# Optimization experiments

Measured on AMD Instinct MI355X. Metric: run time of the kernel, lower is better.

The kernel has to match this reference:

```python
import jax, jax.numpy as jnp
import numpy as np

N_NODES = 50000
N_EDGES = 1600000
NFEAT, NHID, NCLASS = 256, 128, 40
DROPOUT_P = 0.5


def gcn_conv(x, W, b, src, dst, n):
    # PyG GCNConv: h = X W; add self-loops; symmetric norm D^-1/2 (A+I) D^-1/2.
    h = x @ W  # [N, out]
    loop = jnp.arange(n, dtype=src.dtype)
    s = jnp.concatenate([src, loop])  # [E+N]
    d = jnp.concatenate([dst, loop])
    deg = jax.ops.segment_sum(jnp.ones_like(d, dtype=h.dtype), d, num_segments=n)  # in-degree incl. self-loop
    dinv = jax.lax.rsqrt(jnp.maximum(deg, 1.0))
    norm = dinv[s] * dinv[d]  # [E+N]
    msg = h[s] * norm[:, None]  # [E+N, out] gather
    out = jax.ops.segment_sum(msg, d, num_segments=n)  # scatter-add
    return out + b


def setup_inputs() -> dict:
    key = jax.random.key(0)
    k = jax.random.split(key, 7)
    x = jax.random.normal(k[0], (N_NODES, NFEAT), dtype=jnp.float32)
    edge_index = jax.random.randint(k[1], (2, N_EDGES), 0, N_NODES, dtype=jnp.int64)
    W1 = jax.random.normal(k[2], (NFEAT, NHID), dtype=jnp.float32) * (1.0 / np.sqrt(NFEAT))
    b1 = jnp.zeros((NHID,), dtype=jnp.float32)
    W2 = jax.random.normal(k[3], (NHID, NCLASS), dtype=jnp.float32) * (1.0 / np.sqrt(NHID))
    b2 = jnp.zeros((NCLASS,), dtype=jnp.float32)
    keep = jax.random.bernoulli(k[4], 1.0 - DROPOUT_P, (N_NODES, NHID))
    drop_mask = keep.astype(jnp.float32) / (1.0 - DROPOUT_P)  # fixed training-mode dropout mask
    return {"x": x, "edge_index": edge_index, "W1": W1, "b1": b1, "W2": W2, "b2": b2, "drop_mask": drop_mask}


def reference(x, edge_index, W1, b1, W2, b2, drop_mask):
    src, dst = edge_index[0], edge_index[1]
    h = gcn_conv(x, W1, b1, src, dst, N_NODES)
    h = jax.nn.relu(h)
    h = h * drop_mask  # F.dropout(training=True) with fixed mask
    h = gcn_conv(h, W2, b2, src, dst, N_NODES)
    return jax.nn.log_softmax(h, axis=1)
```

## Files before the change

### kernel.cpp

```cpp
#include <hip/hip_runtime.h>
#include <hip/hip_fp16.h>
#include <math.h>

#define N_NODES 50000
#define N_EDGES 1600000
#define NFEAT 256
#define NHID 128
#define NCLASS 40

#define BSHIFT 7
#define NBUCK 391
#define CAP 5120
#define EPB 4096

typedef _Float16 f16x8 __attribute__((ext_vector_type(8)));
typedef float f32x4 __attribute__((ext_vector_type(4)));

__global__ __launch_bounds__(256) void k_binA(const int* __restrict__ src,
                                              const int* __restrict__ dst,
                                              int* __restrict__ gcur,
                                              unsigned int* __restrict__ packed) {
    __shared__ int lhist[NBUCK];
    __shared__ int lbase[NBUCK];
    __shared__ int lcur[NBUCK];
    int t = threadIdx.x;
    for (int i = t; i < NBUCK; i += 256) { lhist[i] = 0; lcur[i] = 0; }
    __syncthreads();
    int e0 = blockIdx.x * EPB;
    int e1 = min(e0 + EPB, N_EDGES);
    for (int e = e0 + t; e < e1; e += 256) {
        int b = dst[e] >> BSHIFT;
        atomicAdd(&lhist[b], 1);
    }
    __syncthreads();
    for (int i = t; i < NBUCK; i += 256)
        lbase[i] = atomicAdd(&gcur[i], lhist[i]);
    __syncthreads();
    for (int e = e0 + t; e < e1; e += 256) {
        int d = dst[e];
        int b = d >> BSHIFT;
        int r = atomicAdd(&lcur[b], 1);
        int pos = lbase[b] + r;
        if (pos < CAP)
            packed[(size_t)b * CAP + pos] =
                ((unsigned int)src[e] << BSHIFT) | (unsigned int)(d & 127);
    }
}

__global__ __launch_bounds__(256) void k_binB(const int* __restrict__ gcur,
                                              const unsigned int* __restrict__ packed,
                                              int* __restrict__ esrc,
                                              int* __restrict__ row_beg,
                                              int* __restrict__ row_cnt,
                                              float* __restrict__ dinv) {
    __shared__ unsigned int sp[CAP];
    __shared__ int hist[128];
    __shared__ int scan[128];
    __shared__ int cur[128];
    int b = blockIdx.x;
    int t = threadIdx.x;
    int cnt = min(gcur[b], CAP);
    if (t < 128) { hist[t] = 0; cur[t] = 0; }
    __syncthreads();
    const unsigned int* pin = packed + (size_t)b * CAP;
    for (int i = t; i < cnt; i += 256) {
        unsigned int w = pin[i];
        sp[i] = w;
        atomicAdd(&hist[w & 127], 1);
    }
    __syncthreads();
    if (t == 0) {
        int s = 0;
        for (int i = 0; i < 128; i++) { scan[i] = s; s += hist[i]; }
    }
    __syncthreads();
    for (int i = t; i < cnt; i += 256) {
        unsigned int w = sp[i];
        int dl = (int)(w & 127u);
        int r = atomicAdd(&cur[dl], 1);
        esrc[(size_t)b * CAP + scan[dl] + r] = (int)(w >> BSHIFT);
    }
    if (t < 128) {
        int node = b * 128 + t;
        if (node < N_NODES) {
            row_beg[node] = b * CAP + scan[t];
            row_cnt[node] = hist[t];
            dinv[node] = rsqrtf((float)(hist[t] + 1));
        }
    }
}

__global__ __launch_bounds__(256) void k_prep(const float* __restrict__ W1,
                                              const float* __restrict__ W2,
                                              __half* __restrict__ w1t,
                                              __half* __restrict__ w2t,
                                              int* __restrict__ gcur) {
    int t = blockIdx.x * 256 + threadIdx.x;
    if (t < NBUCK) gcur[t] = 0;
    if (t < 128 * 256) {
        int n = t >> 8, k = t & 255;
        w1t[t] = __float2half(W1[k * NHID + n]);
    }
    if (t < 48 * 128) {
        int n = t >> 7, k = t & 127;
        w2t[t] = __float2half(n < NCLASS ? W2[k * NCLASS + n] : 0.0f);
    }
}

#define G1_LDA 72
#define G1_LDB 72
#define G1_LDE 136
__global__ __launch_bounds__(256) void k_gemm1(const float* __restrict__ x,
                                               const __half* __restrict__ w1t,
                                               __half* __restrict__ h1h) {
    __shared__ __half smem[64 * G1_LDA + 128 * G1_LDB];
    __half* sA = smem;
    __half* sB = smem + 64 * G1_LDA;
    int t = threadIdx.x;
    int rbase = blockIdx.x * 64;
    int lane = t & 63, wv = t >> 6;
    int m = lane & 15, quad = lane >> 4;
    f32x4 acc[8];
    #pragma unroll
    for (int i = 0; i < 8; i++) acc[i] = (f32x4)0.0f;

    int arow = t >> 2, aseg = t & 3;
    int grow = rbase + arow;
    bool avalid = grow < N_NODES;
    int bn = t >> 1, bseg = t & 1;

    for (int k0 = 0; k0 < NFEAT; k0 += 64) {
        const float4* gs = (const float4*)(x + (size_t)grow * NFEAT + k0 + aseg * 16);
        __half* ad = sA + arow * G1_LDA + aseg * 16;
        #pragma unroll
        for (int i = 0; i < 4; i++) {
            float4 v = avalid ? gs[i] : make_float4(0.f, 0.f, 0.f, 0.f);
            __half2 h0 = __float22half2_rn(make_float2(v.x, v.y));
            __half2 h1 = __float22half2_rn(make_float2(v.z, v.w));
            uint2 st;
            st.x = __builtin_bit_cast(unsigned int, h0);
            st.y = __builtin_bit_cast(unsigned int, h1);
            *(uint2*)(ad + i * 4) = st;
        }
        const uint4* ws4 = (const uint4*)(w1t + bn * NFEAT + k0 + bseg * 32);
        uint4* bd = (uint4*)(sB + bn * G1_LDB + bseg * 32);
        #pragma unroll
        for (int i = 0; i < 4; i++) bd[i] = ws4[i];
        __syncthreads();
        #pragma unroll
        for (int kk = 0; kk < 64; kk += 32) {
            f16x8 af = *(const f16x8*)(sA + (wv * 16 + m) * G1_LDA + kk + quad * 8);
            #pragma unroll
            for (int t8 = 0; t8 < 8; t8++) {
                f16x8 bf = *(const f16x8*)(sB + (t8 * 16 + m) * G1_LDB + kk + quad * 8);
                acc[t8] = __builtin_amdgcn_mfma_f32_16x16x32_f16(af, bf, acc[t8], 0, 0, 0);
            }
        }
        __syncthreads();
    }
    __half* eb = smem;
    #pragma unroll
    for (int t8 = 0; t8 < 8; t8++) {
        #pragma unroll
        for (int r = 0; r < 4; r++)
            eb[(wv * 16 + quad * 4 + r) * G1_LDE + t8 * 16 + m] = __float2half(acc[t8][r]);
    }
    __syncthreads();
    if (avalid) {
        const uint4* es = (const uint4*)(eb + arow * G1_LDE + aseg * 32);
        uint4* od = (uint4*)(h1h + (size_t)grow * NHID + aseg * 32);
        #pragma unroll
        for (int i = 0; i < 4; i++) od[i] = es[i];
    }
}

#define G2_LDA 136
#define G2_LDB 136
#define G2_LDE 72
__global__ __launch_bounds__(256) void k_gemm2(const __half* __restrict__ h1p,
                                               const __half* __restrict__ w2t,
                                               __half* __restrict__ h2p) {
    __shared__ __half smem[64 * G2_LDA + 48 * G2_LDB];
    __half* sA = smem;
    __half* sB = smem + 64 * G2_LDA;
    int t = threadIdx.x;
    int rbase = blockIdx.x * 64;
    int lane = t & 63, wv = t >> 6;
    int m = lane & 15, quad = lane >> 4;
    f32x4 acc[3];
    #pragma unroll
    for (int i = 0; i < 3; i++) acc[i] = (f32x4)0.0f;

    int arow = t >> 2, aseg = t & 3;
    int grow = rbase + arow;
    bool avalid = grow < N_NODES;

    #pragma unroll
    for (int i = 0; i < 3; i++) {
        int idx = t + i * 256;
        int n = idx >> 4, seg = idx & 15;
        *(uint4*)(sB + n * G2_LDB + seg * 8) = *(const uint4*)(w2t + n * NHID + seg * 8);
    }
    {
        const uint4* gs = (const uint4*)(h1p + (size_t)grow * NHID + aseg * 32);
        uint4* ad = (uint4*)(sA + arow * G2_LDA + aseg * 32);
        uint4 z; z.x = z.y = z.z = z.w = 0;
        #pragma unroll
        for (int i = 0; i < 4; i++) ad[i] = avalid ? gs[i] : z;
    }
    __syncthreads();
    #pragma unroll
    for (int kk = 0; kk < 128; kk += 32) {
        f16x8 af = *(const f16x8*)(sA + (wv * 16 + m) * G2_LDA + kk + quad * 8);
        #pragma unroll
        for (int t3 = 0; t3 < 3; t3++) {
            f16x8 bf = *(const f16x8*)(sB + (t3 * 16 + m) * G2_LDB + kk + quad * 8);
            acc[t3] = __builtin_amdgcn_mfma_f32_16x16x32_f16(af, bf, acc[t3], 0, 0, 0);
        }
    }
    __syncthreads();
    __half* eb = smem;
    #pragma unroll
    for (int t3 = 0; t3 < 3; t3++) {
        #pragma unroll
        for (int r = 0; r < 4; r++)
            eb[(wv * 16 + quad * 4 + r) * G2_LDE + t3 * 16 + m] = __float2half(acc[t3][r]);
    }
    {
        int zr = t >> 2, zc = 48 + (t & 3) * 4;
        uint2 z; z.x = z.y = 0;
        *(uint2*)(eb + zr * G2_LDE + zc) = z;
    }
    __syncthreads();
    #pragma unroll
    for (int i = 0; i < 2; i++) {
        int idx = t + i * 256;
        int row = idx >> 3, seg = idx & 7;
        int gr = rbase + row;
        if (gr < N_NODES)
            *(uint4*)(h2p + (size_t)gr * 64 + seg * 8) = *(const uint4*)(eb + row * G2_LDE + seg * 8);
    }
}

__device__ __forceinline__ void acc8f(float* acc, uint4 v, float d) {
    float2 a0 = __half22float2(__builtin_bit_cast(__half2, v.x));
    float2 a1 = __half22float2(__builtin_bit_cast(__half2, v.y));
    float2 a2 = __half22float2(__builtin_bit_cast(__half2, v.z));
    float2 a3 = __half22float2(__builtin_bit_cast(__half2, v.w));
    acc[0] = fmaf(a0.x, d, acc[0]); acc[1] = fmaf(a0.y, d, acc[1]);
    acc[2] = fmaf(a1.x, d, acc[2]); acc[3] = fmaf(a1.y, d, acc[3]);
    acc[4] = fmaf(a2.x, d, acc[4]); acc[5] = fmaf(a2.y, d, acc[5]);
    acc[6] = fmaf(a3.x, d, acc[6]); acc[7] = fmaf(a3.y, d, acc[7]);
}

__global__ __launch_bounds__(64) void k_agg1(const __half* __restrict__ h1h,
                                             const float* __restrict__ dinv,
                                             const int* __restrict__ row_beg,
                                             const int* __restrict__ row_cnt,
                                             const int* __restrict__ esrc,
                                             const float* __restrict__ b1,
                                             const float* __restrict__ mask,
                                             __half* __restrict__ h1p) {
    int i = blockIdx.x;
    int lane = threadIdx.x;
    int q = lane >> 4;
    int fl = lane & 15;
    const uint4* hv4 = (const uint4*)h1h;
    float di = dinv[i];
    __half2 hacc[4];
    __half2 hz = __half2half2(__float2half(0.0f));
    hacc[0] = hz; hacc[1] = hz; hacc[2] = hz; hacc[3] = hz;
    int s0 = row_beg[i], cnt = row_cnt[i];
    for (int base = 0; base < cnt; base += 64) {
        int idx = base + lane;
        int sv = (idx < cnt) ? esrc[s0 + idx] : 0;
        float dv = (idx < cnt) ? dinv[sv] : 0.0f;
        int n = min(64, cnt - base);
        int nr = (n + 31) & ~31;
        for (int j = 0; j < nr; j += 32) {
            int ss[8]; __half2 dd[8]; uint4 vv[8];
            #pragma unroll
            for (int k = 0; k < 8; k++) {
                int jx = j + 4 * k + q;
                ss[k] = __shfl(sv, jx);
                float df = __shfl(dv, jx);
                dd[k] = __half2half2(__float2half(df));
            }
            #pragma unroll
            for (int k = 0; k < 8; k++) vv[k] = hv4[(size_t)ss[k] * 16 + fl];
            #pragma unroll
            for (int k = 0; k < 8; k++) {
                hacc[0] = __hfma2(__builtin_bit_cast(__half2, vv[k].x), dd[k], hacc[0]);
                hacc[1] = __hfma2(__builtin_bit_cast(__half2, vv[k].y), dd[k], hacc[1]);
                hacc[2] = __hfma2(__builtin_bit_cast(__half2, vv[k].z), dd[k], hacc[2]);
                hacc[3] = __hfma2(__builtin_bit_cast(__half2, vv[k].w), dd[k], hacc[3]);
            }
        }
    }
    float acc[8];
    #pragma unroll
    for (int k2 = 0; k2 < 4; k2++) {
        float2 f = __half22float2(hacc[k2]);
        acc[2 * k2] = f.x; acc[2 * k2 + 1] = f.y;
    }
    #pragma unroll
    for (int k = 0; k < 8; k++) {
        acc[k] += __shfl_xor(acc[k], 16);
        acc[k] += __shfl_xor(acc[k], 32);
    }
    if (q == 0) {
        uint4 sv4 = hv4[(size_t)i * 16 + fl];
        acc8f(acc, sv4, di);
        float4 bb0 = ((const float4*)b1)[fl * 2];
        float4 bb1 = ((const float4*)b1)[fl * 2 + 1];
        const float4* mrow = (const float4*)(mask + (size_t)i * NHID);
        float4 mm0 = mrow[fl * 2];
        float4 mm1 = mrow[fl * 2 + 1];
        float o0 = fmaxf(fmaf(acc[0], di, bb0.x), 0.f) * mm0.x;
        float o1 = fmaxf(fmaf(acc[1], di, bb0.y), 0.f) * mm0.y;
        float o2 = fmaxf(fmaf(acc[2], di, bb0.z), 0.f) * mm0.z;
        float o3 = fmaxf(fmaf(acc[3], di, bb0.w), 0.f) * mm0.w;
        float o4 = fmaxf(fmaf(acc[4], di, bb1.x), 0.f) * mm1.x;
        float o5 = fmaxf(fmaf(acc[5], di, bb1.y), 0.f) * mm1.y;
        float o6 = fmaxf(fmaf(acc[6], di, bb1.z), 0.f) * mm1.z;
        float o7 = fmaxf(fmaf(acc[7], di, bb1.w), 0.f) * mm1.w;
        __half2 p0 = __float22half2_rn(make_float2(o0, o1));
        __half2 p1 = __float22half2_rn(make_float2(o2, o3));
        __half2 p2 = __float22half2_rn(make_float2(o4, o5));
        __half2 p3 = __float22half2_rn(make_float2(o6, o7));
        uint4 st;
        st.x = __builtin_bit_cast(unsigned int, p0);
        st.y = __builtin_bit_cast(unsigned int, p1);
        st.z = __builtin_bit_cast(unsigned int, p2);
        st.w = __builtin_bit_cast(unsigned int, p3);
        ((uint4*)h1p)[(size_t)i * 16 + fl] = st;
    }
}

__global__ __launch_bounds__(64) void k_agg2(const __half* __restrict__ h2p,
                                             const float* __restrict__ dinv,
                                             const int* __restrict__ row_beg,
                                             const int* __restrict__ row_cnt,
                                             const int* __restrict__ esrc,
                                             const float* __restrict__ b2,
                                             float* __restrict__ out) {
    int i = blockIdx.x;
    int lane = threadIdx.x;
    int o8 = lane >> 3;
    int fl = lane & 7;
    const uint4* hv4 = (const uint4*)h2p;
    float di = dinv[i];
    __half2 hacc[4];
    __half2 hz = __half2half2(__float2half(0.0f));
    hacc[0] = hz; hacc[1] = hz; hacc[2] = hz; hacc[3] = hz;
    int s0 = row_beg[i], cnt = row_cnt[i];
    for (int base = 0; base < cnt; base += 64) {
        int idx = base + lane;
        int sv = (idx < cnt) ? esrc[s0 + idx] : 0;
        float dv = (idx < cnt) ? dinv[sv] : 0.0f;
        int n = min(64, cnt - base);
        int nr = (n + 31) & ~31;
        for (int j = 0; j < nr; j += 32) {
            int ss[4]; __half2 dd[4]; uint4 vv[4];
            #pragma unroll
            for (int k = 0; k < 4; k++) {
                int jx = j + 8 * k + o8;
                ss[k] = __shfl(sv, jx);
                float df = __shfl(dv, jx);
                dd[k] = __half2half2(__float2half(df));
            }
            #pragma unroll
            for (int k = 0; k < 4; k++) vv[k] = hv4[(size_t)ss[k] * 8 + fl];
            #pragma unroll
            for (int k = 0; k < 4; k++) {
                hacc[0] = __hfma2(__builtin_bit_cast(__half2, vv[k].x), dd[k], hacc[0]);
                hacc[1] = __hfma2(__builtin_bit_cast(__half2, vv[k].y), dd[k], hacc[1]);
                hacc[2] = __hfma2(__builtin_bit_cast(__half2, vv[k].z), dd[k], hacc[2]);
                hacc[3] = __hfma2(__builtin_bit_cast(__half2, vv[k].w), dd[k], hacc[3]);
            }
        }
    }
    float acc[8];
    #pragma unroll
    for (int k2 = 0; k2 < 4; k2++) {
        float2 f = __half22float2(hacc[k2]);
        acc[2 * k2] = f.x; acc[2 * k2 + 1] = f.y;
    }
    if (o8 == 0) {
        uint4 sv4 = hv4[(size_t)i * 8 + fl];
        acc8f(acc, sv4, di);
    }
    #pragma unroll
    for (int k = 0; k < 8; k++) {
        acc[k] += __shfl_xor(acc[k], 8);
        acc[k] += __shfl_xor(acc[k], 16);
        acc[k] += __shfl_xor(acc[k], 32);
    }
    if (o8 == 0) {
        bool act = (fl < 5);
        float val[8];
        float m = -INFINITY;
        if (act) {
            float4 bb0 = ((const float4*)b2)[fl * 2];
            float4 bb1 = ((const float4*)b2)[fl * 2 + 1];
            val[0] = fmaf(acc[0], di, bb0.x);
            val[1] = fmaf(acc[1], di, bb0.y);
            val[2] = fmaf(acc[2], di, bb0.z);
            val[3] = fmaf(acc[3], di, bb0.w);
            val[4] = fmaf(acc[4], di, bb1.x);
            val[5] = fmaf(acc[5], di, bb1.y);
            val[6] = fmaf(acc[6], di, bb1.z);
            val[7] = fmaf(acc[7], di, bb1.w);
            #pragma unroll
            for (int k = 0; k < 8; k++) m = fmaxf(m, val[k]);
        }
        m = fmaxf(m, __shfl_xor(m, 1));
        m = fmaxf(m, __shfl_xor(m, 2));
        m = fmaxf(m, __shfl_xor(m, 4));
        float ss = 0.f;
        if (act) {
            #pragma unroll
            for (int k = 0; k < 8; k++) ss += expf(val[k] - m);
        }
        ss += __shfl_xor(ss, 1);
        ss += __shfl_xor(ss, 2);
        ss += __shfl_xor(ss, 4);
        if (act) {
            float ls = m + logf(ss);
            float4 r0 = make_float4(val[0] - ls, val[1] - ls, val[2] - ls, val[3] - ls);
            float4 r1 = make_float4(val[4] - ls, val[5] - ls, val[6] - ls, val[7] - ls);
            float4* orow = (float4*)(out + (size_t)i * NCLASS + fl * 8);
            orow[0] = r0;
            orow[1] = r1;
        }
    }
}

extern "C" void kernel_launch(void* const* d_in, const int* in_sizes, int n_in,
                              void* d_out, int out_size, void* d_ws, size_t ws_size,
                              hipStream_t stream) {
    const float* x    = (const float*)d_in[0];
    const int*   ei   = (const int*)d_in[1];
    const float* W1   = (const float*)d_in[2];
    const float* b1   = (const float*)d_in[3];
    const float* W2   = (const float*)d_in[4];
    const float* b2   = (const float*)d_in[5];
    const float* mask = (const float*)d_in[6];
    float* out = (float*)d_out;

    const int* src = ei;
    const int* dst = ei + N_EDGES;

    char* ws = (char*)d_ws;
    size_t off = 0;
    __half* h1p    = (__half*)(ws + off); off += (size_t)N_NODES * NHID * 2;
    __half* h1h    = (__half*)(ws + off); off += (size_t)N_NODES * NHID * 2;
    int*    esrc   = (int*)   (ws + off); off += (size_t)NBUCK * CAP * 4;
    float*  dinv   = (float*) (ws + off); off += 200192;
    int*   row_beg = (int*)   (ws + off); off += 200192;
    int*   row_cnt = (int*)   (ws + off); off += 200192;
    int*   gcur    = (int*)   (ws + off); off += 2048;
    __half* w1t    = (__half*)(ws + off); off += 128 * 256 * 2;
    __half* w2t    = (__half*)(ws + off); off += 48 * 128 * 2;

    unsigned int* packed = (unsigned int*)h1p;
    __half* h2p = h1h;

    k_prep<<<128, 256, 0, stream>>>(W1, W2, w1t, w2t, gcur);
    k_binA<<<(N_EDGES + EPB - 1) / EPB, 256, 0, stream>>>(src, dst, gcur, packed);
    k_binB<<<NBUCK, 256, 0, stream>>>(gcur, packed, esrc, row_beg, row_cnt, dinv);

    k_gemm1<<<(N_NODES + 63) / 64, 256, 0, stream>>>(x, w1t, h1h);
    k_agg1<<<N_NODES, 64, 0, stream>>>(h1h, dinv, row_beg, row_cnt, esrc, b1, mask, h1p);
    k_gemm2<<<(N_NODES + 63) / 64, 256, 0, stream>>>(h1p, w2t, h2p);
    k_agg2<<<N_NODES, 64, 0, stream>>>(h2p, dinv, row_beg, row_cnt, esrc, b2, out);
}
```

Baseline: 266.8 us.

## Compact edge indices to 16-bit, shrink bins, and store layer-2 features unpadded

Edge source ids are now stored as unsigned short instead of int, since node ids fit in 16 bits; this halves CSR index traffic in both aggregation kernels. Binning uses 64-node buckets with smaller per-bucket capacity, which reduces shared memory in the second binning pass. The layer-2 hidden matrix is written with a 40-half row stride instead of padding to 64, so agg2 gathers 5 vector loads per neighbour instead of 8 and leaves three lanes per group idle. The main risk is bucket overflow, since each bucket now has less absolute slack above its expected edge count.

```diff
diff --git a/kernel.cpp b/kernel.cpp
--- a/kernel.cpp
+++ b/kernel.cpp
@@ -8,10 +8,10 @@
 #define NHID 128
 #define NCLASS 40
 
-#define BSHIFT 7
-#define NBUCK 391
-#define CAP 5120
-#define EPB 4096
+#define BSHIFT 6
+#define NBUCK 782
+#define CAP 2560
+#define EPB 2048
 
 typedef _Float16 f16x8 __attribute__((ext_vector_type(8)));
 typedef float f32x4 __attribute__((ext_vector_type(4)));
@@ -43,45 +43,45 @@
         int pos = lbase[b] + r;
         if (pos < CAP)
             packed[(size_t)b * CAP + pos] =
-                ((unsigned int)src[e] << BSHIFT) | (unsigned int)(d & 127);
+                ((unsigned int)src[e] << BSHIFT) | (unsigned int)(d & 63);
     }
 }
 
 __global__ __launch_bounds__(256) void k_binB(const int* __restrict__ gcur,
                                               const unsigned int* __restrict__ packed,
-                                              int* __restrict__ esrc,
+                                              unsigned short* __restrict__ esrc,
                                               int* __restrict__ row_beg,
                                               int* __restrict__ row_cnt,
                                               float* __restrict__ dinv) {
     __shared__ unsigned int sp[CAP];
-    __shared__ int hist[128];
-    __shared__ int scan[128];
-    __shared__ int cur[128];
+    __shared__ int hist[64];
+    __shared__ int scan[64];
+    __shared__ int cur[64];
     int b = blockIdx.x;
     int t = threadIdx.x;
     int cnt = min(gcur[b], CAP);
-    if (t < 128) { hist[t] = 0; cur[t] = 0; }
+    if (t < 64) { hist[t] = 0; cur[t] = 0; }
     __syncthreads();
     const unsigned int* pin = packed + (size_t)b * CAP;
     for (int i = t; i < cnt; i += 256) {
         unsigned int w = pin[i];
         sp[i] = w;
-        atomicAdd(&hist[w & 127], 1);
+        atomicAdd(&hist[w & 63], 1);
     }
     __syncthreads();
     if (t == 0) {
         int s = 0;
-        for (int i = 0; i < 128; i++) { scan[i] = s; s += hist[i]; }
+        for (int i = 0; i < 64; i++) { scan[i] = s; s += hist[i]; }
     }
     __syncthreads();
     for (int i = t; i < cnt; i += 256) {
         unsigned int w = sp[i];
-        int dl = (int)(w & 127u);
+        int dl = (int)(w & 63u);
         int r = atomicAdd(&cur[dl], 1);
-        esrc[(size_t)b * CAP + scan[dl] + r] = (int)(w >> BSHIFT);
-    }
-    if (t < 128) {
-        int node = b * 128 + t;
+        esrc[(size_t)b * CAP + scan[dl] + r] = (unsigned short)(w >> BSHIFT);
+    }
+    if (t < 64) {
+        int node = b * 64 + t;
         if (node < N_NODES) {
             row_beg[node] = b * CAP + scan[t];
             row_cnt[node] = hist[t];
@@ -176,7 +176,7 @@
 
 #define G2_LDA 136
 #define G2_LDB 136
-#define G2_LDE 72
+#define G2_LDE 40
 __global__ __launch_bounds__(256) void k_gemm2(const __half* __restrict__ h1p,
                                                const __half* __restrict__ w2t,
                                                __half* __restrict__ h2p) {
@@ -222,23 +222,20 @@
     __half* eb = smem;
     #pragma unroll
     for (int t3 = 0; t3 < 3; t3++) {
-        #pragma unroll
-        for (int r = 0; r < 4; r++)
-            eb[(wv * 16 + quad * 4 + r) * G2_LDE + t3 * 16 + m] = __float2half(acc[t3][r]);
-    }
-    {
-        int zr = t >> 2, zc = 48 + (t & 3) * 4;
-        uint2 z; z.x = z.y = 0;
-        *(uint2*)(eb + zr * G2_LDE + zc) = z;
-    }
-    __syncthreads();
-    #pragma unroll
-    for (int i = 0; i < 2; i++) {
-        int idx = t + i * 256;
-        int row = idx >> 3, seg = idx & 7;
+        int col = t3 * 16 + m;
+        if (col < NCLASS) {
+            #pragma unroll
+            for (int r = 0; r < 4; r++)
+                eb[(wv * 16 + quad * 4 + r) * G2_LDE + col] = __float2half(acc[t3][r]);
+        }
+    }
+    __syncthreads();
+    for (int idx = t; idx < 320; idx += 256) {
+        int row = idx / 5, seg = idx % 5;
         int gr = rbase + row;
         if (gr < N_NODES)
-            *(uint4*)(h2p + (size_t)gr * 64 + seg * 8) = *(const uint4*)(eb + row * G2_LDE + seg * 8);
+            *(uint4*)(h2p + (size_t)gr * G2_LDE + seg * 8) =
+                *(const uint4*)(eb + row * G2_LDE + seg * 8);
     }
 }
 
@@ -257,7 +254,7 @@
                                              const float* __restrict__ dinv,
                                              const int* __restrict__ row_beg,
                                              const int* __restrict__ row_cnt,
-                                             const int* __restrict__ esrc,
+                                             const unsigned short* __restrict__ esrc,
                                              const float* __restrict__ b1,
                                              const float* __restrict__ mask,
                                              __half* __restrict__ h1p) {
@@ -273,7 +270,7 @@
     int s0 = row_beg[i], cnt = row_cnt[i];
     for (int base = 0; base < cnt; base += 64) {
         int idx = base + lane;
-        int sv = (idx < cnt) ? esrc[s0 + idx] : 0;
+        int sv = (idx < cnt) ? (int)esrc[s0 + idx] : 0;
         float dv = (idx < cnt) ? dinv[sv] : 0.0f;
         int n = min(64, cnt - base);
         int nr = (n + 31) & ~31;
@@ -341,22 +338,24 @@
                                              const float* __restrict__ dinv,
                                              const int* __restrict__ row_beg,
                                              const int* __restrict__ row_cnt,
-                                             const int* __restrict__ esrc,
+                                             const unsigned short* __restrict__ esrc,
                                              const float* __restrict__ b2,
                                              float* __restrict__ out) {
     int i = blockIdx.x;
     int lane = threadIdx.x;
     int o8 = lane >> 3;
     int fl = lane & 7;
+    bool gact = fl < 5;
     const uint4* hv4 = (const uint4*)h2p;
     float di = dinv[i];
     __half2 hacc[4];
     __half2 hz = __half2half2(__float2half(0.0f));
     hacc[0] = hz; hacc[1] = hz; hacc[2] = hz; hacc[3] = hz;
     int s0 = row_beg[i], cnt = row_cnt[i];
+    uint4 zero4; zero4.x = zero4.y = zero4.z = zero4.w = 0;
     for (int base = 0; base < cnt; base += 64) {
         int idx = base + lane;
-        int sv = (idx < cnt) ? esrc[s0 + idx] : 0;
+        int sv = (idx < cnt) ? (int)esrc[s0 + idx] : 0;
         float dv = (idx < cnt) ? dinv[sv] : 0.0f;
         int n = min(64, cnt - base);
         int nr = (n + 31) & ~31;
@@ -370,7 +369,7 @@
                 dd[k] = __half2half2(__float2half(df));
             }
             #pragma unroll
-            for (int k = 0; k < 4; k++) vv[k] = hv4[(size_t)ss[k] * 8 + fl];
+            for (int k = 0; k < 4; k++) vv[k] = gact ? hv4[(size_t)ss[k] * 5 + fl] : zero4;
             #pragma unroll
             for (int k = 0; k < 4; k++) {
                 hacc[0] = __hfma2(__builtin_bit_cast(__half2, vv[k].x), dd[k], hacc[0]);
@@ -386,8 +385,8 @@
         float2 f = __half22float2(hacc[k2]);
         acc[2 * k2] = f.x; acc[2 * k2 + 1] = f.y;
     }
-    if (o8 == 0) {
-        uint4 sv4 = hv4[(size_t)i * 8 + fl];
+    if (o8 == 0 && gact) {
+        uint4 sv4 = hv4[(size_t)i * 5 + fl];
         acc8f(acc, sv4, di);
     }
     #pragma unroll
@@ -455,11 +454,12 @@
     size_t off = 0;
     __half* h1p    = (__half*)(ws + off); off += (size_t)N_NODES * NHID * 2;
     __half* h1h    = (__half*)(ws + off); off += (size_t)N_NODES * NHID * 2;
-    int*    esrc   = (int*)   (ws + off); off += (size_t)NBUCK * CAP * 4;
+    unsigned short* esrc = (unsigned short*)(ws + off);
+    off += ((size_t)NBUCK * CAP * 2 + 255) & ~(size_t)255;
     float*  dinv   = (float*) (ws + off); off += 200192;
     int*   row_beg = (int*)   (ws + off); off += 200192;
     int*   row_cnt = (int*)   (ws + off); off += 200192;
-    int*   gcur    = (int*)   (ws + off); off += 2048;
+    int*   gcur    = (int*)   (ws + off); off += 4096;
     __half* w1t    = (__half*)(ws + off); off += 128 * 256 * 2;
     __half* w2t    = (__half*)(ws + off); off += 48 * 128 * 2;
 
```

Result: slower. 282.2 us (+5.7%).

## Segment edges by source range and batch 64 nodes per agg1 block

Applied to the files above, without the earlier changes.

k_binB now sorts each bucket's edges twice. One order groups them by source-node segment (4 ranges of 12800 nodes) and then by destination row. The other is the plain per-row order used by k_agg2. Edge source indices are stored as 16-bit values, halving index traffic. k_agg1 now runs 256-thread blocks covering 64 nodes, with 4 nodes per 16-lane group, walking the segments in order. The aim is to keep the gathered h1 rows within a smaller working set that stays in cache. In exchange, binning does more work, k_agg1 keeps fewer loads in flight per group, and segment locality only holds if blocks progress roughly in step.

```diff
diff --git a/kernel.cpp b/kernel.cpp
--- a/kernel.cpp
+++ b/kernel.cpp
@@ -12,6 +12,8 @@
 #define NBUCK 391
 #define CAP 5120
 #define EPB 4096
+#define SEGN 4
+#define SEGSZ 12800
 
 typedef _Float16 f16x8 __attribute__((ext_vector_type(8)));
 typedef float f32x4 __attribute__((ext_vector_type(4)));
@@ -49,44 +51,89 @@
 
 __global__ __launch_bounds__(256) void k_binB(const int* __restrict__ gcur,
                                               const unsigned int* __restrict__ packed,
-                                              int* __restrict__ esrc,
+                                              unsigned short* __restrict__ esrc_seg,
+                                              unsigned short* __restrict__ esrc_row,
+                                              int* __restrict__ sbeg,
+                                              int* __restrict__ scnt,
                                               int* __restrict__ row_beg,
                                               int* __restrict__ row_cnt,
                                               float* __restrict__ dinv) {
     __shared__ unsigned int sp[CAP];
-    __shared__ int hist[128];
-    __shared__ int scan[128];
-    __shared__ int cur[128];
+    __shared__ int hist[512];
+    __shared__ int scan[512];
+    __shared__ int cur[512];
+    __shared__ int psum[64];
     int b = blockIdx.x;
     int t = threadIdx.x;
     int cnt = min(gcur[b], CAP);
-    if (t < 128) { hist[t] = 0; cur[t] = 0; }
+    for (int i = t; i < 512; i += 256) { hist[i] = 0; cur[i] = 0; }
     __syncthreads();
     const unsigned int* pin = packed + (size_t)b * CAP;
     for (int i = t; i < cnt; i += 256) {
         unsigned int w = pin[i];
         sp[i] = w;
-        atomicAdd(&hist[w & 127], 1);
+        int srcv = (int)(w >> BSHIFT);
+        atomicAdd(&hist[(srcv / SEGSZ) * 128 + (int)(w & 127u)], 1);
+    }
+    __syncthreads();
+    if (t < 64) {
+        int s = 0;
+        #pragma unroll
+        for (int j = 0; j < 8; j++) s += hist[t * 8 + j];
+        psum[t] = s;
     }
     __syncthreads();
     if (t == 0) {
         int s = 0;
-        for (int i = 0; i < 128; i++) { scan[i] = s; s += hist[i]; }
+        for (int j = 0; j < 64; j++) { int v = psum[j]; psum[j] = s; s += v; }
+    }
+    __syncthreads();
+    if (t < 64) {
+        int s = psum[t];
+        #pragma unroll
+        for (int j = 0; j < 8; j++) { scan[t * 8 + j] = s; s += hist[t * 8 + j]; }
+    }
+    __syncthreads();
+    for (int i = t; i < cnt; i += 256) {
+        unsigned int w = sp[i];
+        int srcv = (int)(w >> BSHIFT);
+        int key = (srcv / SEGSZ) * 128 + (int)(w & 127u);
+        int r = atomicAdd(&cur[key], 1);
+        esrc_seg[(size_t)b * CAP + scan[key] + r] = (unsigned short)srcv;
+    }
+    if (t < 128) {
+        int node = b * 128 + t;
+        if (node < N_NODES) {
+            int tot = 0;
+            #pragma unroll
+            for (int s = 0; s < SEGN; s++) {
+                sbeg[node * 4 + s] = b * CAP + scan[s * 128 + t];
+                scnt[node * 4 + s] = hist[s * 128 + t];
+                tot += hist[s * 128 + t];
+            }
+            row_cnt[node] = tot;
+            dinv[node] = rsqrtf((float)(tot + 1));
+        }
+    }
+    __syncthreads();
+    if (t < 128) { hist[t] = 0; cur[t] = 0; }
+    __syncthreads();
+    for (int i = t; i < cnt; i += 256) atomicAdd(&hist[sp[i] & 127u], 1);
+    __syncthreads();
+    if (t == 0) {
+        int s = 0;
+        for (int j = 0; j < 128; j++) { int v = hist[j]; scan[j] = s; s += v; }
     }
     __syncthreads();
     for (int i = t; i < cnt; i += 256) {
         unsigned int w = sp[i];
         int dl = (int)(w & 127u);
         int r = atomicAdd(&cur[dl], 1);
-        esrc[(size_t)b * CAP + scan[dl] + r] = (int)(w >> BSHIFT);
+        esrc_row[(size_t)b * CAP + scan[dl] + r] = (unsigned short)(w >> BSHIFT);
     }
     if (t < 128) {
         int node = b * 128 + t;
-        if (node < N_NODES) {
-            row_beg[node] = b * CAP + scan[t];
-            row_cnt[node] = hist[t];
-            dinv[node] = rsqrtf((float)(hist[t] + 1));
-        }
+        if (node < N_NODES) row_beg[node] = b * CAP + scan[t];
     }
 }
 
@@ -253,69 +300,89 @@
     acc[6] = fmaf(a3.x, d, acc[6]); acc[7] = fmaf(a3.y, d, acc[7]);
 }
 
-__global__ __launch_bounds__(64) void k_agg1(const __half* __restrict__ h1h,
-                                             const float* __restrict__ dinv,
-                                             const int* __restrict__ row_beg,
-                                             const int* __restrict__ row_cnt,
-                                             const int* __restrict__ esrc,
-                                             const float* __restrict__ b1,
-                                             const float* __restrict__ mask,
-                                             __half* __restrict__ h1p) {
-    int i = blockIdx.x;
-    int lane = threadIdx.x;
-    int q = lane >> 4;
-    int fl = lane & 15;
+__global__ __launch_bounds__(256) void k_agg1(const __half* __restrict__ h1h,
+                                              const float* __restrict__ dinv,
+                                              const int* __restrict__ sbeg,
+                                              const int* __restrict__ scnt,
+                                              const unsigned short* __restrict__ esrc_seg,
+                                              const float* __restrict__ b1,
+                                              const float* __restrict__ mask,
+                                              __half* __restrict__ h1p) {
+    int t = threadIdx.x;
+    int qw = t >> 4, ln = t & 15;
+    int nbase = blockIdx.x * 64;
     const uint4* hv4 = (const uint4*)h1h;
-    float di = dinv[i];
-    __half2 hacc[4];
+    __half2 hacc[4][4];
     __half2 hz = __half2half2(__float2half(0.0f));
-    hacc[0] = hz; hacc[1] = hz; hacc[2] = hz; hacc[3] = hz;
-    int s0 = row_beg[i], cnt = row_cnt[i];
-    for (int base = 0; base < cnt; base += 64) {
-        int idx = base + lane;
-        int sv = (idx < cnt) ? esrc[s0 + idx] : 0;
-        float dv = (idx < cnt) ? dinv[sv] : 0.0f;
-        int n = min(64, cnt - base);
-        int nr = (n + 31) & ~31;
-        for (int j = 0; j < nr; j += 32) {
-            int ss[8]; __half2 dd[8]; uint4 vv[8];
-            #pragma unroll
-            for (int k = 0; k < 8; k++) {
-                int jx = j + 4 * k + q;
-                ss[k] = __shfl(sv, jx);
-                float df = __shfl(dv, jx);
-                dd[k] = __half2half2(__float2half(df));
+    #pragma unroll
+    for (int k = 0; k < 4; k++) {
+        hacc[k][0] = hz; hacc[k][1] = hz; hacc[k][2] = hz; hacc[k][3] = hz;
+    }
+    for (int s = 0; s < SEGN; s++) {
+        #pragma unroll
+        for (int k = 0; k < 4; k++) {
+            int node = nbase + qw * 4 + k;
+            if (node >= N_NODES) continue;
+            int beg = sbeg[node * 4 + s];
+            int cn = scnt[node * 4 + s];
+            for (int e0 = 0; e0 < cn; e0 += 16) {
+                int idx = e0 + ln;
+                int sv = (idx < cn) ? (int)esrc_seg[beg + idx] : 0;
+                float dv = (idx < cn) ? dinv[sv] : 0.0f;
+                int n4 = min(16, cn - e0);
+                n4 = (n4 + 3) & ~3;
+                for (int j = 0; j < n4; j += 4) {
+                    int base = qw * 16 + j;
+                    int sA = __shfl(sv, base + 0); float dA = __shfl(dv, base + 0);
+                    int sB = __shfl(sv, base + 1); float dB = __shfl(dv, base + 1);
+                    int sC = __shfl(sv, base + 2); float dC = __shfl(dv, base + 2);
+                    int sD = __shfl(sv, base + 3); float dD = __shfl(dv, base + 3);
+                    uint4 vA = hv4[(size_t)sA * 16 + ln];
+                    uint4 vB = hv4[(size_t)sB * 16 + ln];
+                    uint4 vC = hv4[(size_t)sC * 16 + ln];
+                    uint4 vD = hv4[(size_t)sD * 16 + ln];
+                    __half2 hA = __half2half2(__float2half(dA));
+                    __half2 hB = __half2half2(__float2half(dB));
+                    __half2 hC = __half2half2(__float2half(dC));
+                    __half2 hD = __half2half2(__float2half(dD));
+                    hacc[k][0] = __hfma2(__builtin_bit_cast(__half2, vA.x), hA, hacc[k][0]);
+                    hacc[k][1] = __hfma2(__builtin_bit_cast(__half2, vA.y), hA, hacc[k][1]);
+                    hacc[k][2] = __hfma2(__builtin_bit_cast(__half2, vA.z), hA, hacc[k][2]);
+                    hacc[k][3] = __hfma2(__builtin_bit_cast(__half2, vA.w), hA, hacc[k][3]);
+                    hacc[k][0] = __hfma2(__builtin_bit_cast(__half2, vB.x), hB, hacc[k][0]);
+                    hacc[k][1] = __hfma2(__builtin_bit_cast(__half2, vB.y), hB, hacc[k][1]);
+                    hacc[k][2] = __hfma2(__builtin_bit_cast(__half2, vB.z), hB, hacc[k][2]);
+                    hacc[k][3] = __hfma2(__builtin_bit_cast(__half2, vB.w), hB, hacc[k][3]);
+                    hacc[k][0] = __hfma2(__builtin_bit_cast(__half2, vC.x), hC, hacc[k][0]);
+                    hacc[k][1] = __hfma2(__builtin_bit_cast(__half2, vC.y), hC, hacc[k][1]);
+                    hacc[k][2] = __hfma2(__builtin_bit_cast(__half2, vC.z), hC, hacc[k][2]);
+                    hacc[k][3] = __hfma2(__builtin_bit_cast(__half2, vC.w), hC, hacc[k][3]);
+                    hacc[k][0] = __hfma2(__builtin_bit_cast(__half2, vD.x), hD, hacc[k][0]);
+                    hacc[k][1] = __hfma2(__builtin_bit_cast(__half2, vD.y), hD, hacc[k][1]);
+                    hacc[k][2] = __hfma2(__builtin_bit_cast(__half2, vD.z), hD, hacc[k][2]);
+                    hacc[k][3] = __hfma2(__builtin_bit_cast(__half2, vD.w), hD, hacc[k][3]);
+                }
             }
-            #pragma unroll
-            for (int k = 0; k < 8; k++) vv[k] = hv4[(size_t)ss[k] * 16 + fl];
-            #pragma unroll
-            for (int k = 0; k < 8; k++) {
-                hacc[0] = __hfma2(__builtin_bit_cast(__half2, vv[k].x), dd[k], hacc[0]);
-                hacc[1] = __hfma2(__builtin_bit_cast(__half2, vv[k].y), dd[k], hacc[1]);
-                hacc[2] = __hfma2(__builtin_bit_cast(__half2, vv[k].z), dd[k], hacc[2]);
-                hacc[3] = __hfma2(__builtin_bit_cast(__half2, vv[k].w), dd[k], hacc[3]);
-            }
-        }
-    }
-    float acc[8];
-    #pragma unroll
-    for (int k2 = 0; k2 < 4; k2++) {
-        float2 f = __half22float2(hacc[k2]);
-        acc[2 * k2] = f.x; acc[2 * k2 + 1] = f.y;
-    }
-    #pragma unroll
-    for (int k = 0; k < 8; k++) {
-        acc[k] += __shfl_xor(acc[k], 16);
-        acc[k] += __shfl_xor(acc[k], 32);
-    }
-    if (q == 0) {
-        uint4 sv4 = hv4[(size_t)i * 16 + fl];
+        }
+    }
+    #pragma unroll
+    for (int k = 0; k < 4; k++) {
+        int node = nbase + qw * 4 + k;
+        if (node >= N_NODES) continue;
+        float di = dinv[node];
+        float acc[8];
+        #pragma unroll
+        for (int k2 = 0; k2 < 4; k2++) {
+            float2 f = __half22float2(hacc[k][k2]);
+            acc[2 * k2] = f.x; acc[2 * k2 + 1] = f.y;
+        }
+        uint4 sv4 = hv4[(size_t)node * 16 + ln];
         acc8f(acc, sv4, di);
-        float4 bb0 = ((const float4*)b1)[fl * 2];
-        float4 bb1 = ((const float4*)b1)[fl * 2 + 1];
-        const float4* mrow = (const float4*)(mask + (size_t)i * NHID);
-        float4 mm0 = mrow[fl * 2];
-        float4 mm1 = mrow[fl * 2 + 1];
+        float4 bb0 = ((const float4*)b1)[ln * 2];
+        float4 bb1 = ((const float4*)b1)[ln * 2 + 1];
+        const float4* mrow = (const float4*)(mask + (size_t)node * NHID);
+        float4 mm0 = mrow[ln * 2];
+        float4 mm1 = mrow[ln * 2 + 1];
         float o0 = fmaxf(fmaf(acc[0], di, bb0.x), 0.f) * mm0.x;
         float o1 = fmaxf(fmaf(acc[1], di, bb0.y), 0.f) * mm0.y;
         float o2 = fmaxf(fmaf(acc[2], di, bb0.z), 0.f) * mm0.z;
@@ -333,7 +400,7 @@
         st.y = __builtin_bit_cast(unsigned int, p1);
         st.z = __builtin_bit_cast(unsigned int, p2);
         st.w = __builtin_bit_cast(unsigned int, p3);
-        ((uint4*)h1p)[(size_t)i * 16 + fl] = st;
+        ((uint4*)h1p)[(size_t)node * 16 + ln] = st;
     }
 }
 
@@ -341,7 +408,7 @@
                                              const float* __restrict__ dinv,
                                              const int* __restrict__ row_beg,
                                              const int* __restrict__ row_cnt,
-                                             const int* __restrict__ esrc,
+                                             const unsigned short* __restrict__ esrc,
                                              const float* __restrict__ b2,
                                              float* __restrict__ out) {
     int i = blockIdx.x;
@@ -356,7 +423,7 @@
     int s0 = row_beg[i], cnt = row_cnt[i];
     for (int base = 0; base < cnt; base += 64) {
         int idx = base + lane;
-        int sv = (idx < cnt) ? esrc[s0 + idx] : 0;
+        int sv = (idx < cnt) ? (int)esrc[s0 + idx] : 0;
         float dv = (idx < cnt) ? dinv[sv] : 0.0f;
         int n = min(64, cnt - base);
         int nr = (n + 31) & ~31;
@@ -455,11 +522,16 @@
     size_t off = 0;
     __half* h1p    = (__half*)(ws + off); off += (size_t)N_NODES * NHID * 2;
     __half* h1h    = (__half*)(ws + off); off += (size_t)N_NODES * NHID * 2;
-    int*    esrc   = (int*)   (ws + off); off += (size_t)NBUCK * CAP * 4;
-    float*  dinv   = (float*) (ws + off); off += 200192;
+    unsigned short* esrc_seg = (unsigned short*)(ws + off);
+    off += ((size_t)NBUCK * CAP * 2 + 255) & ~(size_t)255;
+    unsigned short* esrc_row = (unsigned short*)(ws + off);
+    off += ((size_t)NBUCK * CAP * 2 + 255) & ~(size_t)255;
+    int*   sbeg    = (int*)   (ws + off); off += (size_t)N_NODES * 4 * 4;
+    int*   scnt    = (int*)   (ws + off); off += (size_t)N_NODES * 4 * 4;
+    float* dinv    = (float*) (ws + off); off += 200192;
     int*   row_beg = (int*)   (ws + off); off += 200192;
     int*   row_cnt = (int*)   (ws + off); off += 200192;
-    int*   gcur    = (int*)   (ws + off); off += 2048;
+    int*   gcur    = (int*)   (ws + off); off += 4096;
     __half* w1t    = (__half*)(ws + off); off += 128 * 256 * 2;
     __half* w2t    = (__half*)(ws + off); off += 48 * 128 * 2;
 
@@ -468,10 +540,12 @@
 
     k_prep<<<128, 256, 0, stream>>>(W1, W2, w1t, w2t, gcur);
     k_binA<<<(N_EDGES + EPB - 1) / EPB, 256, 0, stream>>>(src, dst, gcur, packed);
-    k_binB<<<NBUCK, 256, 0, stream>>>(gcur, packed, esrc, row_beg, row_cnt, dinv);
+    k_binB<<<NBUCK, 256, 0, stream>>>(gcur, packed, esrc_seg, esrc_row,
+                                      sbeg, scnt, row_beg, row_cnt, dinv);
 
     k_gemm1<<<(N_NODES + 63) / 64, 256, 0, stream>>>(x, w1t, h1h);
-    k_agg1<<<N_NODES, 64, 0, stream>>>(h1h, dinv, row_beg, row_cnt, esrc, b1, mask, h1p);
+    k_agg1<<<(N_NODES + 63) / 64, 256, 0, stream>>>(h1h, dinv, sbeg, scnt,
+                                                    esrc_seg, b1, mask, h1p);
     k_gemm2<<<(N_NODES + 63) / 64, 256, 0, stream>>>(h1p, w2t, h2p);
-    k_agg2<<<N_NODES, 64, 0, stream>>>(h2p, dinv, row_beg, row_cnt, esrc, b2, out);
-}
+    k_agg2<<<N_NODES, 64, 0, stream>>>(h2p, dinv, row_beg, row_cnt, esrc_row, b2, out);
+}
```

After: 278.6 us. 4.4% more time.
